# Performance work log

Measured on AMD Instinct MI355X. Metric: run time of the kernel, lower is better.

## Reference

```python
import jax, jax.numpy as jnp
import numpy as np

ALPHA = 0.6       # blend weight alpha
SEM_W = 0.5       # semantic_weight
PATCH = 3         # patch_size
EPS = 1e-5


def _mean_std(feat):
    # torch .var(dim=2) uses the unbiased estimator (ddof=1)
    N, C = feat.shape[:2]
    f = feat.reshape(N, C, -1)
    var = jnp.var(f, axis=2, ddof=1) + EPS
    return f.mean(axis=2).reshape(N, C, 1, 1), jnp.sqrt(var).reshape(N, C, 1, 1)


def _project(feat):
    m, s = _mean_std(feat)
    return (feat - m) / s


def _unfold(x, p):
    # torch x.unfold(2,p,1).unfold(3,p,1).permute(0,2,3,1,4,5).reshape(-1,C,p,p)
    N, C, H, W = x.shape
    Ho, Wo = H - p + 1, W - p + 1
    pats = jnp.stack([x[:, :, i:i + Ho, j:j + Wo]
                      for i in range(p) for j in range(p)], axis=-1)  # [N,C,Ho,Wo,p*p]
    return pats.transpose(0, 2, 3, 1, 4).reshape(N * Ho * Wo, C, p, p)


def _sgtw(sF, sF_fused, cF_fused, p):
    style_patches = _unfold(sF, p)        # [K, C, p, p]
    fused_patches = _unfold(sF_fused, p)  # [K, Cf, p, p]
    K = fused_patches.shape[0]
    norm = jnp.sqrt(jnp.sum(fused_patches.reshape(K, -1) ** 2, axis=1)).reshape(K, 1, 1, 1)
    kernels = fused_patches / (norm + 1e-7)
    # cross-correlation: content fused features vs normalized style patches
    coord = jax.lax.conv_general_dilated(
        cF_fused, kernels, (1, 1), 'VALID',
        dimension_numbers=('NCHW', 'OIHW', 'NCHW'))  # [N, K, Ho, Wo]
    idx = jnp.argmax(coord, axis=1)       # [N, Ho, Wo] hard top-1 patch match
    # one-hot scatter + conv_transpose2d == gather best patch + overlap-add
    sel = style_patches[idx]              # [N, Ho, Wo, C, p, p]
    N, Ho, Wo = idx.shape
    C = style_patches.shape[1]
    Hout, Wout = Ho + p - 1, Wo + p - 1
    out = jnp.zeros((N, C, Hout, Wout), sel.dtype)
    cnt = jnp.zeros((Hout, Wout), sel.dtype)
    for i in range(p):
        for j in range(p):
            out = out.at[:, :, i:i + Ho, j:j + Wo].add(sel[:, :, :, :, i, j].transpose(0, 3, 1, 2))
            cnt = cnt.at[i:i + Ho, j:j + Wo].add(1.0)
    return out / cnt[None, None]  # overlap-normalized reconstruction


def setup_inputs() -> dict:
    key = jax.random.key(0)
    k1, k2, k3, k4 = jax.random.split(key, 4)
    N, C, Cs, H, W = 1, 512, 64, 64, 64
    return {
        'cF': jax.random.normal(k1, (N, C, H, W), jnp.float32),
        'sF': jax.random.normal(k2, (N, C, H, W), jnp.float32),
        'cF_sem': jax.random.normal(k3, (N, Cs, H, W), jnp.float32),
        'sF_sem': jax.random.normal(k4, (N, Cs, H, W), jnp.float32),
    }


def reference(cF, sF, cF_sem, sF_sem):
    # VSTR_concat
    sF1 = _project(sF)
    cF1 = _project(cF)
    sF_fused = jnp.concatenate([sF1, SEM_W * sF_sem], axis=1)
    cF_fused = jnp.concatenate([cF1, SEM_W * cF_sem], axis=1)
    target = _sgtw(sF, sF_fused, cF_fused, PATCH).reshape(cF.shape)
    return ALPHA * target + (1.0 - ALPHA) * cF
```

## Files before the change

### kernel.cpp

```cpp
#include <hip/hip_runtime.h>
#include <hip/hip_bf16.h>

#define HW      4096
#define WIDTH   64
#define C_MAIN  512
#define C_F     576
#define HO      62
#define KPATCH  3844
#define ALPHA_W 0.6f
#define SEM_W   0.5f
#define EPS_V   1e-5f
#define DELTA   4e-3f

typedef __attribute__((ext_vector_type(8))) short bf16x8;
typedef __attribute__((ext_vector_type(4))) float f32x4;

__global__ __launch_bounds__(256) void stats_kernel(
    const float* __restrict__ cF, const float* __restrict__ sF,
    float4* __restrict__ stats) {
  int b = blockIdx.x;
  int tensor = b >> 9, c = b & 511;
  const float* src = (tensor ? sF : cF) + (size_t)c * HW;
  int t = threadIdx.x;
  float sum = 0.f, sumsq = 0.f;
#pragma unroll
  for (int i = 0; i < 4; ++i) {
    float4 v = *(const float4*)(src + (i * 256 + t) * 4);
    sum   += v.x + v.y + v.z + v.w;
    sumsq += v.x * v.x + v.y * v.y + v.z * v.z + v.w * v.w;
  }
#pragma unroll
  for (int off = 32; off; off >>= 1) {
    sum   += __shfl_down(sum, off, 64);
    sumsq += __shfl_down(sumsq, off, 64);
  }
  __shared__ float ls[8];
  int lane = t & 63, wv = t >> 6;
  if (lane == 0) { ls[wv] = sum; ls[4 + wv] = sumsq; }
  __syncthreads();
  if (t == 0) {
    float s  = ls[0] + ls[1] + ls[2] + ls[3];
    float sq = ls[4] + ls[5] + ls[6] + ls[7];
    float mean = s / 4096.f;
    float var  = (sq - 4096.f * mean * mean) / 4095.f;
    float sig  = sqrtf(var + EPS_V);
    stats[b] = make_float4(mean, 1.f / sig, sig, 0.f);
  }
}

__global__ __launch_bounds__(256) void transform_kernel(
    const float* __restrict__ cF, const float* __restrict__ sF,
    const float* __restrict__ cSem, const float* __restrict__ sSem,
    const float4* __restrict__ stats,
    unsigned short* __restrict__ Ahi, unsigned short* __restrict__ Alo,
    unsigned short* __restrict__ Bhi, unsigned short* __restrict__ Blo,
    float* __restrict__ sFfT) {
  int tensor = blockIdx.z;
  int p0 = blockIdx.x * 32, k0 = blockIdx.y * 32;
  __shared__ float tile[32][33];
  int tx = threadIdx.x & 31, ty = threadIdx.x >> 5;
  for (int r = ty; r < 32; r += 8) {
    int ch = k0 + r;
    float x;
    if (ch < C_MAIN) {
      const float* src = tensor ? sF : cF;
      float4 st = stats[tensor * 512 + ch];
      x = (src[(size_t)ch * HW + p0 + tx] - st.x) * st.y;
    } else {
      const float* src = tensor ? sSem : cSem;
      x = SEM_W * src[(size_t)(ch - C_MAIN) * HW + p0 + tx];
    }
    tile[r][tx] = x;
  }
  __syncthreads();
  unsigned short* dhi = tensor ? Bhi : Ahi;
  unsigned short* dlo = tensor ? Blo : Alo;
  for (int r = ty; r < 32; r += 8) {
    float x = tile[tx][r];
    __hip_bfloat16 hb = __float2bfloat16(x);
    float hf = __bfloat162float(hb);
    __hip_bfloat16 lb = __float2bfloat16(x - hf);
    size_t o = (size_t)(p0 + r) * C_F + k0 + tx;
    dhi[o] = *reinterpret_cast<const unsigned short*>(&hb);
    dlo[o] = *reinterpret_cast<const unsigned short*>(&lb);
    if (tensor) sFfT[o] = x;
  }
}

__global__ __launch_bounds__(256) void gemm_kernel(
    const unsigned short* __restrict__ Ahi, const unsigned short* __restrict__ Alo,
    const unsigned short* __restrict__ Bhi, const unsigned short* __restrict__ Blo,
    float* __restrict__ M) {
  __shared__ __align__(16) unsigned short As_hi[128 * 32];
  __shared__ __align__(16) unsigned short As_lo[128 * 32];
  __shared__ __align__(16) unsigned short Bs_hi[128 * 32];
  __shared__ __align__(16) unsigned short Bs_lo[128 * 32];
  int a0 = blockIdx.x * 128, u0 = blockIdx.y * 128;
  int t = threadIdx.x;
  int lane = t & 63, wave = t >> 6;
  int wr = wave >> 1, wc = wave & 1;
  int l15 = lane & 15, hig = lane >> 4;

  int sr = t >> 2;
  int sc = (t & 3) * 8;
  const unsigned short* Ag0 = Ahi + (size_t)(a0 + sr) * C_F + sc;
  const unsigned short* Ag1 = Alo + (size_t)(a0 + sr) * C_F + sc;
  const unsigned short* Bg0 = Bhi + (size_t)(u0 + sr) * C_F + sc;
  const unsigned short* Bg1 = Blo + (size_t)(u0 + sr) * C_F + sc;
  const size_t rstep = (size_t)64 * C_F;

  uint4 pah0 = *(const uint4*)(Ag0), pah1 = *(const uint4*)(Ag0 + rstep);
  uint4 pal0 = *(const uint4*)(Ag1), pal1 = *(const uint4*)(Ag1 + rstep);
  uint4 pbh0 = *(const uint4*)(Bg0), pbh1 = *(const uint4*)(Bg0 + rstep);
  uint4 pbl0 = *(const uint4*)(Bg1), pbl1 = *(const uint4*)(Bg1 + rstep);

  f32x4 zero4 = {0.f, 0.f, 0.f, 0.f};
  f32x4 acc[4][4];
#pragma unroll
  for (int m = 0; m < 4; ++m)
#pragma unroll
    for (int n = 0; n < 4; ++n) acc[m][n] = zero4;

  int lw = sr * 4 + (t & 3);
  for (int k0 = 0; k0 < C_F; k0 += 32) {
    __syncthreads();
    ((uint4*)As_hi)[lw] = pah0; ((uint4*)As_hi)[lw + 256] = pah1;
    ((uint4*)As_lo)[lw] = pal0; ((uint4*)As_lo)[lw + 256] = pal1;
    ((uint4*)Bs_hi)[lw] = pbh0; ((uint4*)Bs_hi)[lw + 256] = pbh1;
    ((uint4*)Bs_lo)[lw] = pbl0; ((uint4*)Bs_lo)[lw + 256] = pbl1;
    __syncthreads();
    if (k0 + 32 < C_F) {
      Ag0 += 32; Ag1 += 32; Bg0 += 32; Bg1 += 32;
      pah0 = *(const uint4*)(Ag0); pah1 = *(const uint4*)(Ag0 + rstep);
      pal0 = *(const uint4*)(Ag1); pal1 = *(const uint4*)(Ag1 + rstep);
      pbh0 = *(const uint4*)(Bg0); pbh1 = *(const uint4*)(Bg0 + rstep);
      pbl0 = *(const uint4*)(Bg1); pbl1 = *(const uint4*)(Bg1 + rstep);
    }
    bf16x8 bh[4], bl[4];
#pragma unroll
    for (int n = 0; n < 4; ++n) {
      int brow = wc * 64 + n * 16 + l15;
      bh[n] = *(const bf16x8*)&Bs_hi[brow * 32 + hig * 8];
      bl[n] = *(const bf16x8*)&Bs_lo[brow * 32 + hig * 8];
    }
#pragma unroll
    for (int m = 0; m < 4; ++m) {
      int arow = wr * 64 + m * 16 + l15;
      bf16x8 ah = *(const bf16x8*)&As_hi[arow * 32 + hig * 8];
      bf16x8 al = *(const bf16x8*)&As_lo[arow * 32 + hig * 8];
#pragma unroll
      for (int n = 0; n < 4; ++n) {
        acc[m][n] = __builtin_amdgcn_mfma_f32_16x16x32_bf16(ah, bh[n], acc[m][n], 0, 0, 0);
        acc[m][n] = __builtin_amdgcn_mfma_f32_16x16x32_bf16(ah, bl[n], acc[m][n], 0, 0, 0);
        acc[m][n] = __builtin_amdgcn_mfma_f32_16x16x32_bf16(al, bh[n], acc[m][n], 0, 0, 0);
      }
    }
  }
#pragma unroll
  for (int m = 0; m < 4; ++m) {
    int row = a0 + wr * 64 + m * 16 + hig * 4;
#pragma unroll
    for (int n = 0; n < 4; ++n) {
      int col = u0 + wc * 64 + n * 16 + l15;
#pragma unroll
      for (int r = 0; r < 4; ++r)
        M[(size_t)(row + r) * HW + col] = acc[m][n][r];
    }
  }
}

__global__ __launch_bounds__(256) void colsumsq_kernel(
    const float* __restrict__ sFfT, float* __restrict__ q) {
  int row = blockIdx.x * 4 + (threadIdx.x >> 6);
  int lane = threadIdx.x & 63;
  const float* r = sFfT + (size_t)row * C_F;
  float s = 0.f;
  for (int i = lane; i < C_F; i += 64) { float v = r[i]; s += v * v; }
#pragma unroll
  for (int off = 32; off; off >>= 1) s += __shfl_down(s, off, 64);
  if (lane == 0) q[row] = s;
}

__global__ __launch_bounds__(256) void rnorm_kernel(
    const float* __restrict__ q, float* __restrict__ rnorm) {
  int k = blockIdx.x * 256 + threadIdx.x;
  if (k >= KPATCH) return;
  int ky = k / HO, kx = k - ky * HO;
  float s = 0.f;
#pragma unroll
  for (int i = 0; i < 3; ++i)
#pragma unroll
    for (int j = 0; j < 3; ++j) s += q[(ky + i) * WIDTH + kx + j];
  rnorm[k] = 1.f / (sqrtf(s) + 1e-7f);
}

__global__ __launch_bounds__(256) void argmax_kernel(
    const float* __restrict__ M, const float* __restrict__ rnorm,
    const float* __restrict__ sFfT,
    const float* __restrict__ cF, const float* __restrict__ cSem,
    const float4* __restrict__ stats,
    int* __restrict__ idx) {
  int y0 = blockIdx.x * 2, x0 = blockIdx.y * 2;
  int t = threadIdx.x;

  const float* base[4][4];
#pragma unroll
  for (int Y = 0; Y < 4; ++Y)
#pragma unroll
    for (int X = 0; X < 4; ++X)
      base[Y][X] = M + (size_t)((y0 + Y) * WIDTH + x0 + X) * HW;

  float v1[2][2], v2[2][2];
  int   k1[2][2], k2[2][2];
#pragma unroll
  for (int py = 0; py < 2; ++py)
#pragma unroll
    for (int px = 0; px < 2; ++px) {
      v1[py][px] = -1e30f; v2[py][px] = -1e30f;
      k1[py][px] = 0;      k2[py][px] = 0;
    }

  for (int k = t; k < KPATCH; k += 256) {
    int ky = k / HO;
    int u = k + 2 * ky;
    float s[2][2] = {};
#pragma unroll
    for (int i = 0; i < 3; ++i)
#pragma unroll
      for (int j = 0; j < 3; ++j) {
        int col = u + i * WIDTH + j;
#pragma unroll
        for (int py = 0; py < 2; ++py)
#pragma unroll
          for (int px = 0; px < 2; ++px)
            s[py][px] += base[py + i][px + j][col];
      }
    float rn = rnorm[k];
#pragma unroll
    for (int py = 0; py < 2; ++py)
#pragma unroll
      for (int px = 0; px < 2; ++px) {
        float v = s[py][px] * rn;
        if (v > v1[py][px]) {
          v2[py][px] = v1[py][px]; k2[py][px] = k1[py][px];
          v1[py][px] = v;          k1[py][px] = k;
        } else if (v > v2[py][px]) {
          v2[py][px] = v;          k2[py][px] = k;
        }
      }
  }

  __shared__ float sv[256];
  __shared__ int   sk[256];
  __shared__ float redf[256];
  __shared__ float cpatch[9 * C_F];
  __shared__ int   candList[64];
  __shared__ int   candN;
  __shared__ float bestE;
  __shared__ int   bestK;

#pragma unroll
  for (int py = 0; py < 2; ++py)
    for (int px = 0; px < 2; ++px) {
      __syncthreads();
      sv[t] = v1[py][px]; sk[t] = k1[py][px];
      __syncthreads();
      for (int off = 128; off; off >>= 1) {
        if (t < off) {
          float ov = sv[t + off]; int ok = sk[t + off];
          if (ov > sv[t] || (ov == sv[t] && ok < sk[t])) { sv[t] = ov; sk[t] = ok; }
        }
        __syncthreads();
      }
      float vbest = sv[0];
      int   kbest = sk[0];
      float thr = vbest - DELTA;
      if (t == 0) candN = 0;
      __syncthreads();

      if (v2[py][px] >= thr) {
        for (int k = t; k < KPATCH; k += 256) {
          int ky = k / HO;
          int u = k + 2 * ky;
          float s = 0.f;
#pragma unroll
          for (int i = 0; i < 3; ++i)
#pragma unroll
            for (int j = 0; j < 3; ++j)
              s += base[py + i][px + j][u + i * WIDTH + j];
          float v = s * rnorm[k];
          if (v >= thr && k != kbest) {
            int sl = atomicAdd(&candN, 1);
            if (sl < 64) candList[sl] = k;
          }
        }
      } else if (v1[py][px] >= thr && k1[py][px] != kbest) {
        int sl = atomicAdd(&candN, 1);
        if (sl < 64) candList[sl] = k1[py][px];
      }
      __syncthreads();
      int nc = min(candN, 64);
      if (nc == 0) {
        if (t == 0) idx[(y0 + py) * HO + x0 + px] = kbest;
        continue;
      }

      int y = y0 + py, x = x0 + px;
      for (int f = t; f < 9 * C_F; f += 256) {
        int ij = f / C_F, c = f - ij * C_F;
        int pp = (y + ij / 3) * WIDTH + x + ij % 3;
        float cv;
        if (c < C_MAIN) {
          float4 st = stats[c];
          cv = (cF[(size_t)c * HW + pp] - st.x) * st.y;
        } else {
          cv = SEM_W * cSem[(size_t)(c - C_MAIN) * HW + pp];
        }
        cpatch[f] = cv;
      }
      __syncthreads();
      if (t == 0) { bestE = -1e30f; bestK = 0x7fffffff; }
      __syncthreads();

      for (int ci = -1; ci < nc; ++ci) {
        int k = (ci < 0) ? kbest : candList[ci];
        int ky = k / HO, kx = k - ky * HO;
        float part = 0.f;
        for (int f = t; f < 9 * C_F; f += 256) {
          int ij = f / C_F, c = f - ij * C_F;
          int sp = (ky + ij / 3) * WIDTH + kx + ij % 3;
          part += cpatch[f] * sFfT[(size_t)sp * C_F + c];
        }
        redf[t] = part;
        __syncthreads();
        for (int off = 128; off; off >>= 1) {
          if (t < off) redf[t] += redf[t + off];
          __syncthreads();
        }
        if (t == 0) {
          float e = redf[0] * rnorm[k];
          if (e > bestE || (e == bestE && k < bestK)) { bestE = e; bestK = k; }
        }
        __syncthreads();
      }
      if (t == 0) idx[(y0 + py) * HO + x0 + px] = bestK;
    }
}

__global__ __launch_bounds__(256) void gather_kernel(
    const float* __restrict__ sFfT, const int* __restrict__ idx,
    float* __restrict__ tmp) {
  __shared__ int srcs[9];
  __shared__ int nv;
  int pix = blockIdx.x;
  int h = pix >> 6, w = pix & 63;
  if (threadIdx.x == 0) {
    int n = 0;
    for (int i = 0; i < 3; ++i)
      for (int j = 0; j < 3; ++j) {
        int y = h - i, x = w - j;
        if (y >= 0 && y < HO && x >= 0 && x < HO) {
          int k = idx[y * HO + x];
          int ky = k / HO, kx = k - ky * HO;
          srcs[n++] = (ky + i) * WIDTH + kx + j;
        }
      }
    nv = n;
  }
  __syncthreads();
  int n = nv;
  for (int c = threadIdx.x; c < C_MAIN; c += 256) {
    float acc = 0.f;
    for (int s = 0; s < n; ++s) acc += sFfT[(size_t)srcs[s] * C_F + c];
    tmp[(size_t)pix * C_MAIN + c] = acc;
  }
}

__global__ void blend_kernel(
    const float* __restrict__ tmp, const float* __restrict__ cF,
    const float4* __restrict__ stats, float* __restrict__ out) {
  __shared__ float tile[32][33];
  int p0 = blockIdx.x * 32;
  int c0 = blockIdx.y * 32;
  int tx = threadIdx.x, ty = threadIdx.y;
  for (int r = ty; r < 32; r += 8)
    tile[r][tx] = tmp[(size_t)(p0 + r) * C_MAIN + c0 + tx];
  __syncthreads();
  for (int r = ty; r < 32; r += 8) {
    int pix = p0 + tx;
    int h = pix >> 6, w = pix & 63;
    int nh = min(2, h) - max(0, h - 61) + 1;
    int nw = min(2, w) - max(0, w - 61) + 1;
    float inv_cnt = 1.f / (float)(nh * nw);
    int c = c0 + r;
    float4 st = stats[512 + c];
    float recon = st.z * (tile[tx][r] * inv_cnt) + st.x;
    out[(size_t)c * HW + pix] =
        ALPHA_W * recon + (1.f - ALPHA_W) * cF[(size_t)c * HW + pix];
  }
}

extern "C" void kernel_launch(void* const* d_in, const int* in_sizes, int n_in,
                              void* d_out, int out_size, void* d_ws, size_t ws_size,
                              hipStream_t stream) {
  const float* cF   = (const float*)d_in[0];
  const float* sF   = (const float*)d_in[1];
  const float* cSem = (const float*)d_in[2];
  const float* sSem = (const float*)d_in[3];
  float* out = (float*)d_out;

  char* ws = (char*)d_ws;
  unsigned short* Ahi = (unsigned short*)ws;
  unsigned short* Alo = Ahi + (size_t)HW * C_F;
  unsigned short* Bhi = Alo + (size_t)HW * C_F;
  unsigned short* Blo = Bhi + (size_t)HW * C_F;
  float* tmp  = (float*)ws;
  float* M    = (float*)(ws + 18874368);
  float* sFfT = (float*)(ws + 85983232);
  float* q    = (float*)(ws + 95420416);
  float* rnrm = (float*)(ws + 95420416 + 16384);
  int*   idx  = (int*)  (ws + 95420416 + 32768);
  float4* stats = (float4*)(ws + 95420416 + 49152);

  stats_kernel<<<1024, 256, 0, stream>>>(cF, sF, stats);
  transform_kernel<<<dim3(HW / 32, C_F / 32, 2), 256, 0, stream>>>(
      cF, sF, cSem, sSem, stats, Ahi, Alo, Bhi, Blo, sFfT);
  colsumsq_kernel<<<HW / 4, 256, 0, stream>>>(sFfT, q);
  rnorm_kernel<<<(KPATCH + 255) / 256, 256, 0, stream>>>(q, rnrm);
  gemm_kernel<<<dim3(32, 32), 256, 0, stream>>>(Ahi, Alo, Bhi, Blo, M);
  argmax_kernel<<<dim3(31, 31), 256, 0, stream>>>(M, rnrm, sFfT, cF, cSem, stats, idx);
  gather_kernel<<<HW, 256, 0, stream>>>(sFfT, idx, tmp);
  blend_kernel<<<dim3(128, 16), dim3(32, 8), 0, stream>>>(tmp, cF, stats, out);
}
```

Measured before the change: 220.4 us.

## Enlarge argmax pixel tile to 4x4 and load GEMM B operand directly from global

The argmax kernel now handles a 4x4 block of output pixels per workgroup with 512 threads instead of 2x2 with 256. This lets neighbouring pixels share the overlapping 3x3 windows of the correlation matrix M and cuts the number of workgroups. Edge blocks are clamped so they overlap and recompute some pixels, and 16 running top-2 states per thread raise register pressure. Separately, the GEMM kernel drops the LDS staging for the B operand and has each wave read its B fragments straight from global memory. That reduces LDS traffic and synchronisation but gives up reuse of B across waves and the prefetch overlap.

```diff
diff --git a/kernel.cpp b/kernel.cpp
--- a/kernel.cpp
+++ b/kernel.cpp
@@ -93,8 +93,6 @@
     float* __restrict__ M) {
   __shared__ __align__(16) unsigned short As_hi[128 * 32];
   __shared__ __align__(16) unsigned short As_lo[128 * 32];
-  __shared__ __align__(16) unsigned short Bs_hi[128 * 32];
-  __shared__ __align__(16) unsigned short Bs_lo[128 * 32];
   int a0 = blockIdx.x * 128, u0 = blockIdx.y * 128;
   int t = threadIdx.x;
   int lane = t & 63, wave = t >> 6;
@@ -105,14 +103,13 @@
   int sc = (t & 3) * 8;
   const unsigned short* Ag0 = Ahi + (size_t)(a0 + sr) * C_F + sc;
   const unsigned short* Ag1 = Alo + (size_t)(a0 + sr) * C_F + sc;
-  const unsigned short* Bg0 = Bhi + (size_t)(u0 + sr) * C_F + sc;
-  const unsigned short* Bg1 = Blo + (size_t)(u0 + sr) * C_F + sc;
   const size_t rstep = (size_t)64 * C_F;
 
   uint4 pah0 = *(const uint4*)(Ag0), pah1 = *(const uint4*)(Ag0 + rstep);
   uint4 pal0 = *(const uint4*)(Ag1), pal1 = *(const uint4*)(Ag1 + rstep);
-  uint4 pbh0 = *(const uint4*)(Bg0), pbh1 = *(const uint4*)(Bg0 + rstep);
-  uint4 pbl0 = *(const uint4*)(Bg1), pbl1 = *(const uint4*)(Bg1 + rstep);
+
+  const unsigned short* Bg_h = Bhi + (size_t)(u0 + wc * 64 + l15) * C_F + hig * 8;
+  const unsigned short* Bg_l = Blo + (size_t)(u0 + wc * 64 + l15) * C_F + hig * 8;
 
   f32x4 zero4 = {0.f, 0.f, 0.f, 0.f};
   f32x4 acc[4][4];
@@ -123,25 +120,20 @@
 
   int lw = sr * 4 + (t & 3);
   for (int k0 = 0; k0 < C_F; k0 += 32) {
+    bf16x8 bh[4], bl[4];
+#pragma unroll
+    for (int n = 0; n < 4; ++n) {
+      bh[n] = *(const bf16x8*)(Bg_h + (size_t)(n * 16) * C_F + k0);
+      bl[n] = *(const bf16x8*)(Bg_l + (size_t)(n * 16) * C_F + k0);
+    }
     __syncthreads();
     ((uint4*)As_hi)[lw] = pah0; ((uint4*)As_hi)[lw + 256] = pah1;
     ((uint4*)As_lo)[lw] = pal0; ((uint4*)As_lo)[lw + 256] = pal1;
-    ((uint4*)Bs_hi)[lw] = pbh0; ((uint4*)Bs_hi)[lw + 256] = pbh1;
-    ((uint4*)Bs_lo)[lw] = pbl0; ((uint4*)Bs_lo)[lw + 256] = pbl1;
     __syncthreads();
     if (k0 + 32 < C_F) {
-      Ag0 += 32; Ag1 += 32; Bg0 += 32; Bg1 += 32;
+      Ag0 += 32; Ag1 += 32;
       pah0 = *(const uint4*)(Ag0); pah1 = *(const uint4*)(Ag0 + rstep);
       pal0 = *(const uint4*)(Ag1); pal1 = *(const uint4*)(Ag1 + rstep);
-      pbh0 = *(const uint4*)(Bg0); pbh1 = *(const uint4*)(Bg0 + rstep);
-      pbl0 = *(const uint4*)(Bg1); pbl1 = *(const uint4*)(Bg1 + rstep);
-    }
-    bf16x8 bh[4], bl[4];
-#pragma unroll
-    for (int n = 0; n < 4; ++n) {
-      int brow = wc * 64 + n * 16 + l15;
-      bh[n] = *(const bf16x8*)&Bs_hi[brow * 32 + hig * 8];
-      bl[n] = *(const bf16x8*)&Bs_lo[brow * 32 + hig * 8];
     }
 #pragma unroll
     for (int m = 0; m < 4; ++m) {
@@ -194,157 +186,150 @@
   rnorm[k] = 1.f / (sqrtf(s) + 1e-7f);
 }
 
-__global__ __launch_bounds__(256) void argmax_kernel(
+__global__ __launch_bounds__(512) void argmax_kernel(
     const float* __restrict__ M, const float* __restrict__ rnorm,
     const float* __restrict__ sFfT,
     const float* __restrict__ cF, const float* __restrict__ cSem,
     const float4* __restrict__ stats,
     int* __restrict__ idx) {
-  int y0 = blockIdx.x * 2, x0 = blockIdx.y * 2;
+  int y0 = min((int)blockIdx.x * 4, HO - 4);
+  int x0 = min((int)blockIdx.y * 4, HO - 4);
   int t = threadIdx.x;
 
-  const float* base[4][4];
-#pragma unroll
-  for (int Y = 0; Y < 4; ++Y)
-#pragma unroll
-    for (int X = 0; X < 4; ++X)
-      base[Y][X] = M + (size_t)((y0 + Y) * WIDTH + x0 + X) * HW;
-
-  float v1[2][2], v2[2][2];
-  int   k1[2][2], k2[2][2];
-#pragma unroll
-  for (int py = 0; py < 2; ++py)
-#pragma unroll
-    for (int px = 0; px < 2; ++px) {
-      v1[py][px] = -1e30f; v2[py][px] = -1e30f;
-      k1[py][px] = 0;      k2[py][px] = 0;
-    }
-
-  for (int k = t; k < KPATCH; k += 256) {
+  const float* Mbase = M + (size_t)(y0 * WIDTH + x0) * HW;
+  int ijo[9];
+#pragma unroll
+  for (int i = 0; i < 3; ++i)
+#pragma unroll
+    for (int j = 0; j < 3; ++j)
+      ijo[i * 3 + j] = (i * WIDTH + j) * HW + i * WIDTH + j;
+
+  float v1[16], v2[16];
+  int   k1[16], k2[16];
+#pragma unroll
+  for (int p = 0; p < 16; ++p) { v1[p] = -1e30f; v2[p] = -1e30f; k1[p] = 0; k2[p] = 0; }
+
+  for (int k = t; k < KPATCH; k += 512) {
     int ky = k / HO;
     int u = k + 2 * ky;
-    float s[2][2] = {};
-#pragma unroll
-    for (int i = 0; i < 3; ++i)
-#pragma unroll
-      for (int j = 0; j < 3; ++j) {
-        int col = u + i * WIDTH + j;
-#pragma unroll
-        for (int py = 0; py < 2; ++py)
-#pragma unroll
-          for (int px = 0; px < 2; ++px)
-            s[py][px] += base[py + i][px + j][col];
-      }
+    float s[16];
+#pragma unroll
+    for (int p = 0; p < 16; ++p) s[p] = 0.f;
+#pragma unroll
+    for (int o = 0; o < 9; ++o) {
+      const float* p9 = Mbase + ijo[o] + u;
+#pragma unroll
+      for (int py = 0; py < 4; ++py)
+#pragma unroll
+        for (int px = 0; px < 4; ++px)
+          s[py * 4 + px] += p9[(size_t)(py * WIDTH + px) * HW];
+    }
     float rn = rnorm[k];
 #pragma unroll
-    for (int py = 0; py < 2; ++py)
-#pragma unroll
-      for (int px = 0; px < 2; ++px) {
-        float v = s[py][px] * rn;
-        if (v > v1[py][px]) {
-          v2[py][px] = v1[py][px]; k2[py][px] = k1[py][px];
-          v1[py][px] = v;          k1[py][px] = k;
-        } else if (v > v2[py][px]) {
-          v2[py][px] = v;          k2[py][px] = k;
-        }
-      }
-  }
-
-  __shared__ float sv[256];
-  __shared__ int   sk[256];
-  __shared__ float redf[256];
+    for (int p = 0; p < 16; ++p) {
+      float v = s[p] * rn;
+      if (v > v1[p]) { v2[p] = v1[p]; k2[p] = k1[p]; v1[p] = v; k1[p] = k; }
+      else if (v > v2[p]) { v2[p] = v; k2[p] = k; }
+    }
+  }
+
+  __shared__ float sv[512];
+  __shared__ int   sk[512];
+  __shared__ float redf[512];
   __shared__ float cpatch[9 * C_F];
   __shared__ int   candList[64];
   __shared__ int   candN;
   __shared__ float bestE;
   __shared__ int   bestK;
 
-#pragma unroll
-  for (int py = 0; py < 2; ++py)
-    for (int px = 0; px < 2; ++px) {
+  for (int pp = 0; pp < 16; ++pp) {
+    int py = pp >> 2, px = pp & 3;
+    float mv1 = -1e30f, mv2 = -1e30f; int mk1 = 0, mk2 = 0;
+#pragma unroll
+    for (int q = 0; q < 16; ++q)
+      if (q == pp) { mv1 = v1[q]; mv2 = v2[q]; mk1 = k1[q]; mk2 = k2[q]; }
+
+    __syncthreads();
+    sv[t] = mv1; sk[t] = mk1;
+    __syncthreads();
+    for (int off = 256; off; off >>= 1) {
+      if (t < off) {
+        float ov = sv[t + off]; int ok = sk[t + off];
+        if (ov > sv[t] || (ov == sv[t] && ok < sk[t])) { sv[t] = ov; sk[t] = ok; }
+      }
       __syncthreads();
-      sv[t] = v1[py][px]; sk[t] = k1[py][px];
+    }
+    float vbest = sv[0];
+    int   kbest = sk[0];
+    float thr = vbest - DELTA;
+    if (t == 0) candN = 0;
+    __syncthreads();
+
+    int poff = (py * WIDTH + px) * HW;
+    if (mv2 >= thr) {
+      for (int k = t; k < KPATCH; k += 512) {
+        int ky = k / HO;
+        int u = k + 2 * ky;
+        float s = 0.f;
+#pragma unroll
+        for (int o = 0; o < 9; ++o) s += Mbase[(size_t)(poff + ijo[o]) + u];
+        float v = s * rnorm[k];
+        if (v >= thr && k != kbest) {
+          int sl = atomicAdd(&candN, 1);
+          if (sl < 64) candList[sl] = k;
+        }
+      }
+    } else if (mv1 >= thr && mk1 != kbest) {
+      int sl = atomicAdd(&candN, 1);
+      if (sl < 64) candList[sl] = mk1;
+    }
+    __syncthreads();
+    int nc = min(candN, 64);
+    if (nc == 0) {
+      if (t == 0) idx[(y0 + py) * HO + x0 + px] = kbest;
+      continue;
+    }
+
+    int y = y0 + py, x = x0 + px;
+    for (int f = t; f < 9 * C_F; f += 512) {
+      int ij = f / C_F, c = f - ij * C_F;
+      int pp2 = (y + ij / 3) * WIDTH + x + ij % 3;
+      float cv;
+      if (c < C_MAIN) {
+        float4 st = stats[c];
+        cv = (cF[(size_t)c * HW + pp2] - st.x) * st.y;
+      } else {
+        cv = SEM_W * cSem[(size_t)(c - C_MAIN) * HW + pp2];
+      }
+      cpatch[f] = cv;
+    }
+    __syncthreads();
+    if (t == 0) { bestE = -1e30f; bestK = 0x7fffffff; }
+    __syncthreads();
+
+    for (int ci = -1; ci < nc; ++ci) {
+      int k = (ci < 0) ? kbest : candList[ci];
+      int ky = k / HO, kx = k - ky * HO;
+      float part = 0.f;
+      for (int f = t; f < 9 * C_F; f += 512) {
+        int ij = f / C_F, c = f - ij * C_F;
+        int sp = (ky + ij / 3) * WIDTH + kx + ij % 3;
+        part += cpatch[f] * sFfT[(size_t)sp * C_F + c];
+      }
+      redf[t] = part;
       __syncthreads();
-      for (int off = 128; off; off >>= 1) {
-        if (t < off) {
-          float ov = sv[t + off]; int ok = sk[t + off];
-          if (ov > sv[t] || (ov == sv[t] && ok < sk[t])) { sv[t] = ov; sk[t] = ok; }
-        }
+      for (int off = 256; off; off >>= 1) {
+        if (t < off) redf[t] += redf[t + off];
         __syncthreads();
       }
-      float vbest = sv[0];
-      int   kbest = sk[0];
-      float thr = vbest - DELTA;
-      if (t == 0) candN = 0;
+      if (t == 0) {
+        float e = redf[0] * rnorm[k];
+        if (e > bestE || (e == bestE && k < bestK)) { bestE = e; bestK = k; }
+      }
       __syncthreads();
-
-      if (v2[py][px] >= thr) {
-        for (int k = t; k < KPATCH; k += 256) {
-          int ky = k / HO;
-          int u = k + 2 * ky;
-          float s = 0.f;
-#pragma unroll
-          for (int i = 0; i < 3; ++i)
-#pragma unroll
-            for (int j = 0; j < 3; ++j)
-              s += base[py + i][px + j][u + i * WIDTH + j];
-          float v = s * rnorm[k];
-          if (v >= thr && k != kbest) {
-            int sl = atomicAdd(&candN, 1);
-            if (sl < 64) candList[sl] = k;
-          }
-        }
-      } else if (v1[py][px] >= thr && k1[py][px] != kbest) {
-        int sl = atomicAdd(&candN, 1);
-        if (sl < 64) candList[sl] = k1[py][px];
-      }
-      __syncthreads();
-      int nc = min(candN, 64);
-      if (nc == 0) {
-        if (t == 0) idx[(y0 + py) * HO + x0 + px] = kbest;
-        continue;
-      }
-
-      int y = y0 + py, x = x0 + px;
-      for (int f = t; f < 9 * C_F; f += 256) {
-        int ij = f / C_F, c = f - ij * C_F;
-        int pp = (y + ij / 3) * WIDTH + x + ij % 3;
-        float cv;
-        if (c < C_MAIN) {
-          float4 st = stats[c];
-          cv = (cF[(size_t)c * HW + pp] - st.x) * st.y;
-        } else {
-          cv = SEM_W * cSem[(size_t)(c - C_MAIN) * HW + pp];
-        }
-        cpatch[f] = cv;
-      }
-      __syncthreads();
-      if (t == 0) { bestE = -1e30f; bestK = 0x7fffffff; }
-      __syncthreads();
-
-      for (int ci = -1; ci < nc; ++ci) {
-        int k = (ci < 0) ? kbest : candList[ci];
-        int ky = k / HO, kx = k - ky * HO;
-        float part = 0.f;
-        for (int f = t; f < 9 * C_F; f += 256) {
-          int ij = f / C_F, c = f - ij * C_F;
-          int sp = (ky + ij / 3) * WIDTH + kx + ij % 3;
-          part += cpatch[f] * sFfT[(size_t)sp * C_F + c];
-        }
-        redf[t] = part;
-        __syncthreads();
-        for (int off = 128; off; off >>= 1) {
-          if (t < off) redf[t] += redf[t + off];
-          __syncthreads();
-        }
-        if (t == 0) {
-          float e = redf[0] * rnorm[k];
-          if (e > bestE || (e == bestE && k < bestK)) { bestE = e; bestK = k; }
-        }
-        __syncthreads();
-      }
-      if (t == 0) idx[(y0 + py) * HO + x0 + px] = bestK;
-    }
+    }
+    if (t == 0) idx[(y0 + py) * HO + x0 + px] = bestK;
+  }
 }
 
 __global__ __launch_bounds__(256) void gather_kernel(
@@ -428,7 +413,7 @@
   colsumsq_kernel<<<HW / 4, 256, 0, stream>>>(sFfT, q);
   rnorm_kernel<<<(KPATCH + 255) / 256, 256, 0, stream>>>(q, rnrm);
   gemm_kernel<<<dim3(32, 32), 256, 0, stream>>>(Ahi, Alo, Bhi, Blo, M);
-  argmax_kernel<<<dim3(31, 31), 256, 0, stream>>>(M, rnrm, sFfT, cF, cSem, stats, idx);
+  argmax_kernel<<<dim3(16, 16), 512, 0, stream>>>(M, rnrm, sFfT, cF, cSem, stats, idx);
   gather_kernel<<<HW, 256, 0, stream>>>(sFfT, idx, tmp);
   blend_kernel<<<dim3(128, 16), dim3(32, 8), 0, stream>>>(tmp, cF, stats, out);
 }
```

Result: slower. 279.0 us (+26.6%).
